# Optimization experiments

Measured on AMD Instinct MI355X. Metric: run time of the kernel, lower is better.

The kernel has to match this reference:

```python
import jax, jax.numpy as jnp
import numpy as np

# model dims
C_CH = 64      # channels C
M_DIM = 128    # state dim m
R = 8          # low-rank r
DG = 64        # token_dim d_g
CHUNK = 512    # chunk_len
B, H, W = 4, 256, 256


def setup_inputs() -> dict:
    key = jax.random.key(0)
    ks = jax.random.split(key, 12)
    n = jax.random.normal
    return {
        "x": n(ks[0], (B, C_CH, H, W), jnp.float32),
        "g": n(ks[1], (B, DG), jnp.float32),
        # 1x1 conv weights flattened to matrices
        "in_proj_w": n(ks[2], (M_DIM, C_CH), jnp.float32) * 0.05,
        "in_proj_b": jnp.zeros((M_DIM,), jnp.float32),
        "out_proj_w": n(ks[3], (C_CH, M_DIM), jnp.float32) * 0.05,  # Cbase; conv bias unused in forward
        "U_base": n(ks[4], (M_DIM, R), jnp.float32) * 0.02,
        "V_base": n(ks[5], (M_DIM, R), jnp.float32) * 0.02,
        "a_base": jnp.zeros((M_DIM,), jnp.float32),
        "mod_uv_w": n(ks[6], (2 * R, DG), jnp.float32) * 0.05,
        "mod_uv_b": jnp.zeros((2 * R,), jnp.float32),
        "mod_a_w": n(ks[7], (M_DIM, DG), jnp.float32) * 0.05,
        "mod_a_b": jnp.zeros((M_DIM,), jnp.float32),
        "mod_B_w": n(ks[8], (M_DIM, DG), jnp.float32) * 0.05,
        "mod_B_b": jnp.zeros((M_DIM,), jnp.float32),
        "mod_C_w": n(ks[9], (C_CH, DG), jnp.float32) * 0.05,
        "mod_C_b": jnp.zeros((C_CH,), jnp.float32),
        "h0": jnp.zeros((M_DIM,), jnp.float32),
    }


def reference(x, g, in_proj_w, in_proj_b, out_proj_w, U_base, V_base, a_base,
              mod_uv_w, mod_uv_b, mod_a_w, mod_a_b, mod_B_w, mod_B_b,
              mod_C_w, mod_C_b, h0):
    Bsz, Cch, Hh, Ww = x.shape
    # 1x1 conv in_proj
    x_proj = jnp.einsum('bchw,mc->bmhw', x, in_proj_w) + in_proj_b[None, :, None, None]
    # g-conditioned modulations
    uv = g @ mod_uv_w.T + mod_uv_b
    gU = jnp.clip(uv[:, :R], -0.5, 0.5)[:, None, :]          # (B,1,r)
    gV = jnp.clip(uv[:, R:], -0.5, 0.5)[:, None, :]          # (B,1,r)
    ga = jnp.clip(g @ mod_a_w.T + mod_a_b, -2.0, 2.0)        # (B,m)
    gB = jnp.clip(g @ mod_B_w.T + mod_B_b, -1.0, 1.0)        # (B,m)
    gC = jnp.clip(g @ mod_C_w.T + mod_C_b, -0.5, 0.5)        # (B,C)
    Ug = U_base[None] * (1.0 + gU)                            # (B,m,r)
    Vg = V_base[None] * (1.0 + gV)                            # (B,m,r)
    a = a_base[None] + ga                                     # (B,m)
    Cg = out_proj_w[None] * (1.0 + gC)[:, :, None]            # (B,C,m)

    L = Hh * Ww
    x_seq = x_proj.reshape(Bsz, M_DIM, L).transpose(0, 2, 1)  # (B,L,m)
    x_seq = x_seq * (1.0 + gB)[:, None, :]
    pad = (-L) % CHUNK
    if pad > 0:
        x_seq = jnp.pad(x_seq, ((0, 0), (0, pad), (0, 0)))
    Lp = L + pad
    Mch = Lp // CHUNK
    # (T, B, K, m): scan over time within chunks, chunks run in parallel
    x_chunks = x_seq.reshape(Bsz, Mch, CHUNK, M_DIM).transpose(2, 0, 1, 3)
    h_init = jnp.broadcast_to(h0, (Bsz, Mch, M_DIM))

    def step(h, xt):
        v = jnp.einsum('bmr,bkm->bkr', Vg, h)                 # V^T h
        Av = jnp.einsum('bmr,bkr->bkm', Ug, v)                # U (V^T h)
        h_new = jnp.clip(Av + h * a[:, None, :] + xt, -10.0, 10.0)
        yc = jnp.clip(jnp.einsum('bcm,bkm->bkc', Cg, h_new), -10.0, 10.0)
        return h_new, yc

    _, ys = jax.lax.scan(step, h_init, x_chunks)              # (T,B,K,C)
    out_flat = ys.transpose(1, 2, 0, 3).reshape(Bsz, Lp, Cch)[:, :L, :]
    return out_flat.transpose(0, 2, 1).reshape(Bsz, Cch, Hh, Ww)
```

## Files before the change

kernel.cpp:

```cpp
#include <hip/hip_runtime.h>
#include <hip/hip_fp16.h>

#define L_TOT 65536

#define WS_UG   0
#define WS_VG   4096
#define WS_A    8192
#define WS_GB1  8704
#define WS_CGP  32768
#define WS_XS   65536

typedef __attribute__((ext_vector_type(8))) short short8;
typedef __attribute__((ext_vector_type(4))) float f32x4;

__device__ __forceinline__ unsigned bf16rne(float f) {
    unsigned u = __builtin_bit_cast(unsigned, f);
    return (u + 0x7fffu + ((u >> 16) & 1u)) >> 16;
}

#define DPP_ROW(CT) \
    "v_add_f32_dpp %0, %0, %0 " CT "\n\t" \
    "v_add_f32_dpp %1, %1, %1 " CT "\n\t" \
    "v_add_f32_dpp %2, %2, %2 " CT "\n\t" \
    "v_add_f32_dpp %3, %3, %3 " CT "\n\t" \
    "v_add_f32_dpp %4, %4, %4 " CT "\n\t" \
    "v_add_f32_dpp %5, %5, %5 " CT "\n\t" \
    "v_add_f32_dpp %6, %6, %6 " CT "\n\t" \
    "v_add_f32_dpp %7, %7, %7 " CT "\n\t"

__global__ __launch_bounds__(128) void mod_kernel(
    const float* __restrict__ g,
    const float* __restrict__ U_base, const float* __restrict__ V_base,
    const float* __restrict__ a_base, const float* __restrict__ out_proj_w,
    const float* __restrict__ mod_uv_w, const float* __restrict__ mod_uv_b,
    const float* __restrict__ mod_a_w, const float* __restrict__ mod_a_b,
    const float* __restrict__ mod_B_w, const float* __restrict__ mod_B_b,
    const float* __restrict__ mod_C_w, const float* __restrict__ mod_C_b,
    float* __restrict__ ws)
{
    __shared__ float gsh[64];
    __shared__ float uvs[16];
    __shared__ float gCs[64];
    const int b = blockIdx.x, tid = threadIdx.x;
    if (tid < 64) gsh[tid] = g[b * 64 + tid];
    __syncthreads();
    if (tid < 16) {
        float s = mod_uv_b[tid];
        for (int d = 0; d < 64; ++d) s += mod_uv_w[tid * 64 + d] * gsh[d];
        uvs[tid] = fminf(0.5f, fmaxf(-0.5f, s));
    }
    float ga_v, gB_v;
    {
        float s = mod_a_b[tid];
        for (int d = 0; d < 64; ++d) s += mod_a_w[tid * 64 + d] * gsh[d];
        ga_v = fminf(2.0f, fmaxf(-2.0f, s));
    }
    {
        float s = mod_B_b[tid];
        for (int d = 0; d < 64; ++d) s += mod_B_w[tid * 64 + d] * gsh[d];
        gB_v = 1.0f + fminf(1.0f, fmaxf(-1.0f, s));
    }
    if (tid < 64) {
        float s = mod_C_b[tid];
        for (int d = 0; d < 64; ++d) s += mod_C_w[tid * 64 + d] * gsh[d];
        gCs[tid] = 1.0f + fminf(0.5f, fmaxf(-0.5f, s));
    }
    __syncthreads();
    for (int idx = tid; idx < 1024; idx += 128) {
        int m = idx >> 3, r = idx & 7;
        ws[WS_UG + (b * 128 + m) * 8 + r] = U_base[m * 8 + r] * (1.0f + uvs[r]);
        ws[WS_VG + (b * 128 + m) * 8 + r] = V_base[m * 8 + r] * (1.0f + uvs[8 + r]);
    }
    ws[WS_A   + b * 128 + tid] = a_base[tid] + ga_v;
    ws[WS_GB1 + b * 128 + tid] = gB_v;
    unsigned* CgP = (unsigned*)(ws + WS_CGP);
    for (int idx = tid; idx < 4096; idx += 128) {
        int c = idx >> 6, j = idx & 63;
        float s = gCs[c];
        float c0 = out_proj_w[c * 128 + 2 * j]     * s;
        float c1 = out_proj_w[c * 128 + 2 * j + 1] * s;
        CgP[(b * 64 + c) * 64 + j] = bf16rne(c0) | (bf16rne(c1) << 16);
    }
}

__global__ __launch_bounds__(256) void inproj_kernel(
    const float* __restrict__ x, const float* __restrict__ W,
    const float* __restrict__ bias, const float* __restrict__ ws,
    unsigned* __restrict__ xs16)
{
    __shared__ float xsh[64][68];
    __shared__ float Wsh[128][65];
    const int tid = threadIdx.x;
    const int b = blockIdx.y;
    const int l0 = blockIdx.x * 64;

    #pragma unroll
    for (int rep = 0; rep < 4; ++rep) {
        int idx = rep * 256 + tid;
        int c = idx >> 4, p = idx & 15;
        float4 v = *(const float4*)(x + (size_t)(b * 64 + c) * L_TOT + l0 + p * 4);
        *(float4*)&xsh[c][p * 4] = v;
    }
    #pragma unroll
    for (int rep = 0; rep < 8; ++rep) {
        int idx = rep * 256 + tid;
        int m = idx >> 4, c4 = (idx & 15) * 4;
        float4 wv = *(const float4*)(W + m * 64 + c4);
        Wsh[m][c4]     = wv.x;
        Wsh[m][c4 + 1] = wv.y;
        Wsh[m][c4 + 2] = wv.z;
        Wsh[m][c4 + 3] = wv.w;
    }
    const int mp = tid & 63, lq = tid >> 6;
    const int m0 = 2 * mp;
    float acc0[16], acc1[16];
    #pragma unroll
    for (int j = 0; j < 16; ++j) { acc0[j] = 0.0f; acc1[j] = 0.0f; }
    __syncthreads();

    for (int c = 0; c < 64; ++c) {
        float w0 = Wsh[m0][c], w1 = Wsh[m0 + 1][c];
        #pragma unroll
        for (int j4 = 0; j4 < 4; ++j4) {
            float4 xv = *(const float4*)&xsh[c][lq * 16 + j4 * 4];
            acc0[j4 * 4 + 0] = fmaf(w0, xv.x, acc0[j4 * 4 + 0]);
            acc0[j4 * 4 + 1] = fmaf(w0, xv.y, acc0[j4 * 4 + 1]);
            acc0[j4 * 4 + 2] = fmaf(w0, xv.z, acc0[j4 * 4 + 2]);
            acc0[j4 * 4 + 3] = fmaf(w0, xv.w, acc0[j4 * 4 + 3]);
            acc1[j4 * 4 + 0] = fmaf(w1, xv.x, acc1[j4 * 4 + 0]);
            acc1[j4 * 4 + 1] = fmaf(w1, xv.y, acc1[j4 * 4 + 1]);
            acc1[j4 * 4 + 2] = fmaf(w1, xv.z, acc1[j4 * 4 + 2]);
            acc1[j4 * 4 + 3] = fmaf(w1, xv.w, acc1[j4 * 4 + 3]);
        }
    }
    const float gb0 = ws[WS_GB1 + b * 128 + m0];
    const float gb1 = ws[WS_GB1 + b * 128 + m0 + 1];
    const float b0 = bias[m0], b1 = bias[m0 + 1];
    #pragma unroll
    for (int j = 0; j < 16; ++j) {
        int l = l0 + lq * 16 + j;
        float v0 = (acc0[j] + b0) * gb0;
        float v1 = (acc1[j] + b1) * gb1;
        __half2 hp = __floats2half2_rn(v0, v1);
        xs16[((size_t)b * L_TOT + l) * 64 + mp] = __builtin_bit_cast(unsigned, hp);
    }
}

__global__ __launch_bounds__(64, 1) void scan_kernel(
    const unsigned* __restrict__ xs16, const float* __restrict__ ws,
    const unsigned* __restrict__ CgP, const float* __restrict__ h0,
    float* __restrict__ out)
{
    __shared__ __align__(16) unsigned Hs[16 * 68];
    const int lane = threadIdx.x;
    const int bb = blockIdx.x >> 7, k = blockIdx.x & 127;
    const int m0 = 2 * lane;

    float Vg0[8], Vg1[8], Ug0[8], Ug1[8];
    {
        const float* vg = ws + WS_VG + (bb * 128 + m0) * 8;
        const float* ug = ws + WS_UG + (bb * 128 + m0) * 8;
        #pragma unroll
        for (int r = 0; r < 8; ++r) {
            Vg0[r] = vg[r]; Vg1[r] = vg[8 + r];
            Ug0[r] = ug[r]; Ug1[r] = ug[8 + r];
        }
    }
    const float a0 = ws[WS_A + bb * 128 + m0];
    const float a1 = ws[WS_A + bb * 128 + m0 + 1];
    float ha = h0[m0], hb = h0[m0 + 1];

    short8 Af[4][4];
    const int row16 = lane & 15, grp = lane >> 4;
    #pragma unroll
    for (int ct = 0; ct < 4; ++ct)
        #pragma unroll
        for (int kc = 0; kc < 4; ++kc) {
            const unsigned* p = CgP + (bb * 64 + ct * 16 + row16) * 64 + kc * 16 + grp * 4;
            Af[ct][kc] = __builtin_bit_cast(short8, *(const uint4*)p);
        }

    const unsigned* xsp = xs16 + ((size_t)bb * L_TOT + (size_t)k * 512) * 64 + lane;
    float* ob[4];
    #pragma unroll
    for (int ct = 0; ct < 4; ++ct)
        ob[ct] = out + (size_t)(bb * 64 + ct * 16 + grp * 4) * L_TOT + k * 512 + row16;

    unsigned xqA[16], xqB[16];

    auto prefetch = [&](unsigned (&xq)[16], int seg) {
        const unsigned* xb = xsp + (size_t)seg * 1024;
        #pragma unroll
        for (int i = 0; i < 16; ++i) xq[i] = xb[(size_t)i * 64];
    };
    auto do_seg = [&](const unsigned (&xq)[16], int t16) {
        #pragma unroll
        for (int i = 0; i < 16; ++i) {
            const float2 xv = __half22float2(__builtin_bit_cast(__half2, xq[i]));
            float p0 = fmaf(Vg1[0], hb, Vg0[0] * ha);
            float p1 = fmaf(Vg1[1], hb, Vg0[1] * ha);
            float p2 = fmaf(Vg1[2], hb, Vg0[2] * ha);
            float p3 = fmaf(Vg1[3], hb, Vg0[3] * ha);
            float p4 = fmaf(Vg1[4], hb, Vg0[4] * ha);
            float p5 = fmaf(Vg1[5], hb, Vg0[5] * ha);
            float p6 = fmaf(Vg1[6], hb, Vg0[6] * ha);
            float p7 = fmaf(Vg1[7], hb, Vg0[7] * ha);
            asm volatile(
                "s_nop 1\n\t"
                DPP_ROW("quad_perm:[1,0,3,2] row_mask:0xf bank_mask:0xf bound_ctrl:1")
                DPP_ROW("quad_perm:[2,3,0,1] row_mask:0xf bank_mask:0xf bound_ctrl:1")
                DPP_ROW("row_half_mirror row_mask:0xf bank_mask:0xf bound_ctrl:1")
                DPP_ROW("row_mirror row_mask:0xf bank_mask:0xf bound_ctrl:1")
                DPP_ROW("row_bcast:15 row_mask:0xa bank_mask:0xf")
                DPP_ROW("row_bcast:31 row_mask:0xc bank_mask:0xf")
                : "+v"(p0), "+v"(p1), "+v"(p2), "+v"(p3),
                  "+v"(p4), "+v"(p5), "+v"(p6), "+v"(p7));
            float v0 = __builtin_bit_cast(float, __builtin_amdgcn_readlane(__builtin_bit_cast(int, p0), 63));
            float v1 = __builtin_bit_cast(float, __builtin_amdgcn_readlane(__builtin_bit_cast(int, p1), 63));
            float v2 = __builtin_bit_cast(float, __builtin_amdgcn_readlane(__builtin_bit_cast(int, p2), 63));
            float v3 = __builtin_bit_cast(float, __builtin_amdgcn_readlane(__builtin_bit_cast(int, p3), 63));
            float v4 = __builtin_bit_cast(float, __builtin_amdgcn_readlane(__builtin_bit_cast(int, p4), 63));
            float v5 = __builtin_bit_cast(float, __builtin_amdgcn_readlane(__builtin_bit_cast(int, p5), 63));
            float v6 = __builtin_bit_cast(float, __builtin_amdgcn_readlane(__builtin_bit_cast(int, p6), 63));
            float v7 = __builtin_bit_cast(float, __builtin_amdgcn_readlane(__builtin_bit_cast(int, p7), 63));
            float q0 = fmaf(v1, Ug0[1], v0 * Ug0[0]);
            float q1 = fmaf(v3, Ug0[3], v2 * Ug0[2]);
            float q2 = fmaf(v5, Ug0[5], v4 * Ug0[4]);
            float q3 = fmaf(v7, Ug0[7], v6 * Ug0[6]);
            float av0 = (q0 + q1) + (q2 + q3);
            float s0 = fmaf(v1, Ug1[1], v0 * Ug1[0]);
            float s1 = fmaf(v3, Ug1[3], v2 * Ug1[2]);
            float s2 = fmaf(v5, Ug1[5], v4 * Ug1[4]);
            float s3 = fmaf(v7, Ug1[7], v6 * Ug1[6]);
            float av1 = (s0 + s1) + (s2 + s3);
            ha = fminf(10.0f, fmaxf(-10.0f, fmaf(a0, ha, av0) + xv.x));
            hb = fminf(10.0f, fmaxf(-10.0f, fmaf(a1, hb, av1) + xv.y));
            unsigned hp;
            asm("v_cvt_pk_bf16_f32 %0, %1, %2" : "=v"(hp) : "v"(ha), "v"(hb));
            Hs[i * 68 + lane] = hp;
        }
        short8 Bf[4];
        #pragma unroll
        for (int kc = 0; kc < 4; ++kc)
            Bf[kc] = __builtin_bit_cast(short8,
                *(const uint4*)&Hs[row16 * 68 + kc * 16 + grp * 4]);
        #pragma unroll
        for (int ct = 0; ct < 4; ++ct) {
            f32x4 acc = {0.0f, 0.0f, 0.0f, 0.0f};
            #pragma unroll
            for (int kc = 0; kc < 4; ++kc)
                acc = __builtin_amdgcn_mfma_f32_16x16x32_bf16(Af[ct][kc], Bf[kc], acc, 0, 0, 0);
            #pragma unroll
            for (int r = 0; r < 4; ++r) {
                float y = fminf(10.0f, fmaxf(-10.0f, acc[r]));
                ob[ct][(size_t)r * L_TOT + t16 * 16] = y;
            }
        }
    };

    prefetch(xqA, 0);
    #pragma unroll 1
    for (int t16 = 0; t16 < 32; t16 += 2) {
        prefetch(xqB, t16 + 1);
        do_seg(xqA, t16);
        prefetch(xqA, (t16 + 2) & 31);
        do_seg(xqB, t16 + 1);
    }
}

extern "C" void kernel_launch(void* const* d_in, const int* in_sizes, int n_in,
                              void* d_out, int out_size, void* d_ws, size_t ws_size,
                              hipStream_t stream) {
    const float* x          = (const float*)d_in[0];
    const float* g          = (const float*)d_in[1];
    const float* in_proj_w  = (const float*)d_in[2];
    const float* in_proj_b  = (const float*)d_in[3];
    const float* out_proj_w = (const float*)d_in[4];
    const float* U_base     = (const float*)d_in[5];
    const float* V_base     = (const float*)d_in[6];
    const float* a_base     = (const float*)d_in[7];
    const float* mod_uv_w   = (const float*)d_in[8];
    const float* mod_uv_b   = (const float*)d_in[9];
    const float* mod_a_w    = (const float*)d_in[10];
    const float* mod_a_b    = (const float*)d_in[11];
    const float* mod_B_w    = (const float*)d_in[12];
    const float* mod_B_b    = (const float*)d_in[13];
    const float* mod_C_w    = (const float*)d_in[14];
    const float* mod_C_b    = (const float*)d_in[15];
    const float* h0         = (const float*)d_in[16];
    float* out = (float*)d_out;
    float* ws  = (float*)d_ws;
    unsigned* xs16 = (unsigned*)(ws + WS_XS);

    hipLaunchKernelGGL(mod_kernel, dim3(4), dim3(128), 0, stream,
                       g, U_base, V_base, a_base, out_proj_w,
                       mod_uv_w, mod_uv_b, mod_a_w, mod_a_b,
                       mod_B_w, mod_B_b, mod_C_w, mod_C_b, ws);
    hipLaunchKernelGGL(inproj_kernel, dim3(1024, 4), dim3(256), 0, stream,
                       x, in_proj_w, in_proj_b, ws, xs16);
    hipLaunchKernelGGL(scan_kernel, dim3(512), dim3(64), 0, stream,
                       xs16, ws, (const unsigned*)(ws + WS_CGP), h0, out);
}
```

Baseline: 191.7 us.

## Compute 1x1 in_proj with split-bf16 MFMA instead of FP32 FMA loops

Replaces the scalar FP32 in_proj GEMM with a kernel that uses bf16 MFMA 16x16x32 instructions. Precision is kept close to FP32 by splitting the weights and inputs into hi and lo bf16 parts and summing three products. The weight split is precomputed in mod_kernel, and the input split is done into LDS. This is meant to cut the ALU cost of the projection stage. It adds MFMA issue cost and slightly lower precision, and the total may still be dominated by the scan kernel.

```diff
diff --git a/kernel.cpp b/kernel.cpp
--- a/kernel.cpp
+++ b/kernel.cpp
@@ -7,6 +7,8 @@
 #define WS_VG   4096
 #define WS_A    8192
 #define WS_GB1  8704
+#define WS_WHP  12288
+#define WS_WLP  16384
 #define WS_CGP  32768
 #define WS_XS   65536
 
@@ -16,6 +18,9 @@
 __device__ __forceinline__ unsigned bf16rne(float f) {
     unsigned u = __builtin_bit_cast(unsigned, f);
     return (u + 0x7fffu + ((u >> 16) & 1u)) >> 16;
+}
+__device__ __forceinline__ float bfhi(unsigned u) {
+    return __builtin_bit_cast(float, u << 16);
 }
 
 #define DPP_ROW(CT) \
@@ -29,7 +34,7 @@
     "v_add_f32_dpp %7, %7, %7 " CT "\n\t"
 
 __global__ __launch_bounds__(128) void mod_kernel(
-    const float* __restrict__ g,
+    const float* __restrict__ g, const float* __restrict__ in_proj_w,
     const float* __restrict__ U_base, const float* __restrict__ V_base,
     const float* __restrict__ a_base, const float* __restrict__ out_proj_w,
     const float* __restrict__ mod_uv_w, const float* __restrict__ mod_uv_b,
@@ -81,68 +86,97 @@
         float c1 = out_proj_w[c * 128 + 2 * j + 1] * s;
         CgP[(b * 64 + c) * 64 + j] = bf16rne(c0) | (bf16rne(c1) << 16);
     }
-}
-
-__global__ __launch_bounds__(256) void inproj_kernel(
-    const float* __restrict__ x, const float* __restrict__ W,
-    const float* __restrict__ bias, const float* __restrict__ ws,
-    unsigned* __restrict__ xs16)
+    if (b == 0) {
+        unsigned* WhP = (unsigned*)(ws + WS_WHP);
+        unsigned* WlP = (unsigned*)(ws + WS_WLP);
+        for (int idx = tid; idx < 4096; idx += 128) {
+            int m = idx >> 5, j = idx & 31;
+            float w0 = in_proj_w[m * 64 + 2 * j];
+            float w1 = in_proj_w[m * 64 + 2 * j + 1];
+            unsigned u0 = bf16rne(w0), u1 = bf16rne(w1);
+            WhP[idx] = u0 | (u1 << 16);
+            float r0 = w0 - bfhi(u0);
+            float r1 = w1 - bfhi(u1);
+            WlP[idx] = bf16rne(r0) | (bf16rne(r1) << 16);
+        }
+    }
+}
+
+__global__ __launch_bounds__(256) void inproj_mfma(
+    const float* __restrict__ x, const unsigned* __restrict__ WhP,
+    const unsigned* __restrict__ WlP, const float* __restrict__ bias,
+    const float* __restrict__ ws, unsigned* __restrict__ xs16)
 {
-    __shared__ float xsh[64][68];
-    __shared__ float Wsh[128][65];
+    __shared__ __align__(16) unsigned XhS[64 * 36];
+    __shared__ __align__(16) unsigned XlS[64 * 36];
     const int tid = threadIdx.x;
     const int b = blockIdx.y;
     const int l0 = blockIdx.x * 64;
 
+    {
+        const int l_st = tid & 63, cpg = tid >> 6;
+        #pragma unroll
+        for (int s = 0; s < 8; ++s) {
+            int cp = cpg * 8 + s;
+            float x0 = x[(size_t)(b * 64 + 2 * cp) * L_TOT + l0 + l_st];
+            float x1 = x[(size_t)(b * 64 + 2 * cp + 1) * L_TOT + l0 + l_st];
+            unsigned u0 = bf16rne(x0), u1 = bf16rne(x1);
+            XhS[l_st * 36 + cp] = u0 | (u1 << 16);
+            float r0 = x0 - bfhi(u0);
+            float r1 = x1 - bfhi(u1);
+            XlS[l_st * 36 + cp] = bf16rne(r0) | (bf16rne(r1) << 16);
+        }
+    }
+    const int lane = tid & 63, wv = tid >> 6;
+    const int row16 = lane & 15, grp = lane >> 4;
+
+    short8 Ah[2][2], Al[2][2];
     #pragma unroll
-    for (int rep = 0; rep < 4; ++rep) {
-        int idx = rep * 256 + tid;
-        int c = idx >> 4, p = idx & 15;
-        float4 v = *(const float4*)(x + (size_t)(b * 64 + c) * L_TOT + l0 + p * 4);
-        *(float4*)&xsh[c][p * 4] = v;
-    }
+    for (int t = 0; t < 2; ++t) {
+        const int mrow = (2 * wv + t) * 16 + row16;
+        #pragma unroll
+        for (int kc = 0; kc < 2; ++kc) {
+            Ah[t][kc] = __builtin_bit_cast(short8,
+                *(const uint4*)(WhP + mrow * 32 + kc * 16 + grp * 4));
+            Al[t][kc] = __builtin_bit_cast(short8,
+                *(const uint4*)(WlP + mrow * 32 + kc * 16 + grp * 4));
+        }
+    }
+    __syncthreads();
+
     #pragma unroll
-    for (int rep = 0; rep < 8; ++rep) {
-        int idx = rep * 256 + tid;
-        int m = idx >> 4, c4 = (idx & 15) * 4;
-        float4 wv = *(const float4*)(W + m * 64 + c4);
-        Wsh[m][c4]     = wv.x;
-        Wsh[m][c4 + 1] = wv.y;
-        Wsh[m][c4 + 2] = wv.z;
-        Wsh[m][c4 + 3] = wv.w;
-    }
-    const int mp = tid & 63, lq = tid >> 6;
-    const int m0 = 2 * mp;
-    float acc0[16], acc1[16];
-    #pragma unroll
-    for (int j = 0; j < 16; ++j) { acc0[j] = 0.0f; acc1[j] = 0.0f; }
-    __syncthreads();
-
-    for (int c = 0; c < 64; ++c) {
-        float w0 = Wsh[m0][c], w1 = Wsh[m0 + 1][c];
-        #pragma unroll
-        for (int j4 = 0; j4 < 4; ++j4) {
-            float4 xv = *(const float4*)&xsh[c][lq * 16 + j4 * 4];
-            acc0[j4 * 4 + 0] = fmaf(w0, xv.x, acc0[j4 * 4 + 0]);
-            acc0[j4 * 4 + 1] = fmaf(w0, xv.y, acc0[j4 * 4 + 1]);
-            acc0[j4 * 4 + 2] = fmaf(w0, xv.z, acc0[j4 * 4 + 2]);
-            acc0[j4 * 4 + 3] = fmaf(w0, xv.w, acc0[j4 * 4 + 3]);
-            acc1[j4 * 4 + 0] = fmaf(w1, xv.x, acc1[j4 * 4 + 0]);
-            acc1[j4 * 4 + 1] = fmaf(w1, xv.y, acc1[j4 * 4 + 1]);
-            acc1[j4 * 4 + 2] = fmaf(w1, xv.z, acc1[j4 * 4 + 2]);
-            acc1[j4 * 4 + 3] = fmaf(w1, xv.w, acc1[j4 * 4 + 3]);
-        }
-    }
-    const float gb0 = ws[WS_GB1 + b * 128 + m0];
-    const float gb1 = ws[WS_GB1 + b * 128 + m0 + 1];
-    const float b0 = bias[m0], b1 = bias[m0 + 1];
-    #pragma unroll
-    for (int j = 0; j < 16; ++j) {
-        int l = l0 + lq * 16 + j;
-        float v0 = (acc0[j] + b0) * gb0;
-        float v1 = (acc1[j] + b1) * gb1;
-        __half2 hp = __floats2half2_rn(v0, v1);
-        xs16[((size_t)b * L_TOT + l) * 64 + mp] = __builtin_bit_cast(unsigned, hp);
+    for (int ti = 0; ti < 4; ++ti) {
+        const int lcol = ti * 16 + row16;
+        short8 Bh[2], Bl[2];
+        #pragma unroll
+        for (int kc = 0; kc < 2; ++kc) {
+            Bh[kc] = __builtin_bit_cast(short8,
+                *(const uint4*)&XhS[lcol * 36 + kc * 16 + grp * 4]);
+            Bl[kc] = __builtin_bit_cast(short8,
+                *(const uint4*)&XlS[lcol * 36 + kc * 16 + grp * 4]);
+        }
+        #pragma unroll
+        for (int t = 0; t < 2; ++t) {
+            f32x4 acc = {0.f, 0.f, 0.f, 0.f};
+            acc = __builtin_amdgcn_mfma_f32_16x16x32_bf16(Ah[t][0], Bh[0], acc, 0, 0, 0);
+            acc = __builtin_amdgcn_mfma_f32_16x16x32_bf16(Ah[t][1], Bh[1], acc, 0, 0, 0);
+            acc = __builtin_amdgcn_mfma_f32_16x16x32_bf16(Ah[t][0], Bl[0], acc, 0, 0, 0);
+            acc = __builtin_amdgcn_mfma_f32_16x16x32_bf16(Ah[t][1], Bl[1], acc, 0, 0, 0);
+            acc = __builtin_amdgcn_mfma_f32_16x16x32_bf16(Al[t][0], Bh[0], acc, 0, 0, 0);
+            acc = __builtin_amdgcn_mfma_f32_16x16x32_bf16(Al[t][1], Bh[1], acc, 0, 0, 0);
+            const int mb = (2 * wv + t) * 16 + 4 * grp;
+            const int l = l0 + lcol;
+            float4 bi = *(const float4*)(bias + mb);
+            float4 gb = *(const float4*)(ws + WS_GB1 + b * 128 + mb);
+            float v0 = (acc[0] + bi.x) * gb.x;
+            float v1 = (acc[1] + bi.y) * gb.y;
+            float v2 = (acc[2] + bi.z) * gb.z;
+            float v3 = (acc[3] + bi.w) * gb.w;
+            __half2 h01 = __floats2half2_rn(v0, v1);
+            __half2 h23 = __floats2half2_rn(v2, v3);
+            uint2 pk = {__builtin_bit_cast(unsigned, h01), __builtin_bit_cast(unsigned, h23)};
+            *(uint2*)(xs16 + ((size_t)b * L_TOT + l) * 64 + (mb >> 1)) = pk;
+        }
     }
 }
 
@@ -293,11 +327,12 @@
     unsigned* xs16 = (unsigned*)(ws + WS_XS);
 
     hipLaunchKernelGGL(mod_kernel, dim3(4), dim3(128), 0, stream,
-                       g, U_base, V_base, a_base, out_proj_w,
+                       g, in_proj_w, U_base, V_base, a_base, out_proj_w,
                        mod_uv_w, mod_uv_b, mod_a_w, mod_a_b,
                        mod_B_w, mod_B_b, mod_C_w, mod_C_b, ws);
-    hipLaunchKernelGGL(inproj_kernel, dim3(1024, 4), dim3(256), 0, stream,
-                       x, in_proj_w, in_proj_b, ws, xs16);
+    hipLaunchKernelGGL(inproj_mfma, dim3(1024, 4), dim3(256), 0, stream,
+                       x, (const unsigned*)(ws + WS_WHP), (const unsigned*)(ws + WS_WLP),
+                       in_proj_b, ws, xs16);
     hipLaunchKernelGGL(scan_kernel, dim3(512), dim3(64), 0, stream,
                        xs16, ws, (const unsigned*)(ws + WS_CGP), h0, out);
 }
```

After: 172.1 us. -10.2%, faster.
